# Performance work log

Hardware: AMD Instinct MI355X
Metric: run time of the kernel (lower is better)

Reference implementation:

```python
import jax, jax.numpy as jnp
import numpy as np
import math

INPUT_DIM = 128
HIDDEN = 256
SEQ = 512      # former_seq_len
OUT = 24       # output_dim == number of decode steps
TEMP = 64      # temp_node
B = 512


def setup_inputs() -> dict:
    key = jax.random.key(0)
    ks = jax.random.split(key, 13)
    stdv = 1.0 / math.sqrt(HIDDEN)  # matches init_weights: normal(0, stdv)
    p = lambda k, shape: jax.random.normal(k, shape, dtype=jnp.float32) * stdv
    return {
        "H": jax.random.normal(ks[0], (B, SEQ, INPUT_DIM), dtype=jnp.float32),
        "y_0": jax.random.normal(ks[1], (B, 1), dtype=jnp.float32),
        "embedding": jax.random.normal(ks[2], (B, 2 * HIDDEN), dtype=jnp.float32),
        "Wa": p(ks[3], (INPUT_DIM, OUT, TEMP)),
        "Ua": p(ks[4], (HIDDEN, OUT, TEMP)),
        "ba": p(ks[5], (OUT, TEMP)),
        "Va": p(ks[6], (TEMP, OUT, 1)),
        "W": p(ks[7], (INPUT_DIM, OUT, 4 * HIDDEN)),
        "U": p(ks[8], (HIDDEN, OUT, 4 * HIDDEN)),
        "bias": p(ks[9], (OUT, 4 * HIDDEN)),
        "W_y": p(ks[10], (1, OUT, 4 * HIDDEN)),
        "fc_w": p(ks[11], (OUT, HIDDEN)),   # per-step Linear(hidden,1) weights
        "fc_b": p(ks[12], (OUT, 1)),        # per-step Linear biases
    }


def reference(H, y_0, embedding, Wa, Ua, ba, Va, W, U, bias, W_y, fc_w, fc_b):
    HS = HIDDEN
    scale = 1.0 / math.sqrt(HS)
    h0 = embedding[:, :HS]
    c0 = embedding[:, HS:]
    # stack per-timestep weight slices along a leading T axis for lax.scan
    params = (
        jnp.moveaxis(Wa, 1, 0),   # [T, D, TEMP]
        jnp.moveaxis(Ua, 1, 0),   # [T, HS, TEMP]
        ba,                        # [T, TEMP]
        jnp.moveaxis(Va, 1, 0),   # [T, TEMP, 1]
        jnp.moveaxis(W, 1, 0),    # [T, D, 4HS]
        jnp.moveaxis(U, 1, 0),    # [T, HS, 4HS]
        bias,                      # [T, 4HS]
        jnp.moveaxis(W_y, 1, 0),  # [T, 1, 4HS]
        fc_w,                      # [T, HS]
        fc_b,                      # [T, 1]
    )

    def step(carry, p):
        h_t, c_t, y_prev = carry
        Wa_t, Ua_t, ba_t, Va_t, W_t, U_t, b_t, Wy_t, fcw_t, fcb_t = p
        # additive attention over the encoder sequence (note: uses cell state c_t)
        e = jnp.tanh(H @ Wa_t + (c_t @ Ua_t)[:, None, :] + ba_t) @ Va_t  # [B, L, 1]
        beta = jax.nn.softmax(e[..., 0] * scale, axis=1)                 # [B, L]
        ctx = jnp.einsum('bl,bld->bd', beta, H)                          # [B, D]
        gates = ctx @ W_t + h_t @ U_t + b_t + y_prev @ Wy_t              # [B, 4HS]
        i = jax.nn.sigmoid(gates[:, :HS])
        f = jax.nn.sigmoid(gates[:, HS:2 * HS])
        g = jnp.tanh(gates[:, 2 * HS:3 * HS])
        o = jax.nn.sigmoid(gates[:, 3 * HS:])
        c_new = f * c_t + i * g
        h_new = o * jnp.tanh(c_new)
        y = h_new @ fcw_t[:, None] + fcb_t                                # [B, 1]
        return (h_new, c_new, y), (h_new, y[:, 0])

    _, (hs, ys) = jax.lax.scan(step, (h0, c0, y_0), params)
    y_out = jnp.transpose(ys)            # [B, T]
    hidden_seq = jnp.moveaxis(hs, 0, 1)  # [B, T, HS]
    return y_out, hidden_seq
```

## Files before the change

kernel.cpp:

```cpp
#include <hip/hip_runtime.h>
#include <hip/hip_fp8.h>
#include <cstdint>
#include <cstddef>

#define IDIM 128
#define HS   256
#define SEQL 512
#define TOUT 24
#define TMP  64
#define NB   512
#define G4   1024

typedef unsigned short u16;
typedef unsigned int   u32;
typedef __attribute__((ext_vector_type(4))) float f32x4;
typedef _Float16 f16x8 __attribute__((ext_vector_type(8)));

#define OFF_HFRAG 0
#define OFF_GATEP 65536
#define OFF_E     73728
#define OFF_CUAP  75776
#define OFF_H     77824
#define OFF_C     78848
#define OFF_CTX   79872
#define OFF_CUABA 80384
#define OFF_VA    80640
#define OFF_RED   80896
#define OFF_Y     80992
#define OFF_INVD  80996
#define OFF_AB    81000
#define SMEM_BYTES 81768

__device__ __forceinline__ u16 f2bf(float f) {
  union { float f; u32 u; } v; v.f = f;
  u32 r = v.u + 0x7FFFu + ((v.u >> 16) & 1u);
  return (u16)(r >> 16);
}
__device__ __forceinline__ float bflo(u32 u) {
  union { u32 u; float f; } v; v.u = u << 16; return v.f;
}
__device__ __forceinline__ float bfhi(u32 u) {
  union { u32 u; float f; } v; v.u = u & 0xFFFF0000u; return v.f;
}
__device__ __forceinline__ u32 pkbf(float a, float b) {
  return (u32)f2bf(a) | ((u32)f2bf(b) << 16);
}
__device__ __forceinline__ u32 pkf16(float a, float b) {
  union { _Float16 h[2]; u32 u; } v;
  v.h[0] = (_Float16)a; v.h[1] = (_Float16)b; return v.u;
}
__device__ __forceinline__ u32 pk4_fp8(float a, float b, float c, float d) {
#if __has_builtin(__builtin_amdgcn_cvt_pk_fp8_f32)
  u32 v = (u32)__builtin_amdgcn_cvt_pk_fp8_f32(a, b, 0, false);
  v = (u32)__builtin_amdgcn_cvt_pk_fp8_f32(c, d, (int)v, true);
  return v;
#else
  __hip_fp8_e4m3 x(a), y(b), z(c), w(d);
  return (u32)x.__x | ((u32)y.__x << 8) | ((u32)z.__x << 16) | ((u32)w.__x << 24);
#endif
}
template <int S>
__device__ __forceinline__ float fp8_f32(u32 v) {
#if __has_builtin(__builtin_amdgcn_cvt_f32_fp8)
  return __builtin_amdgcn_cvt_f32_fp8((int)v, S);
#else
  __hip_fp8_e4m3 x; x.__x = (unsigned char)(v >> (8 * S)); return (float)x;
#endif
}
__device__ __forceinline__ float tanh_fast(float x) {
  float x2 = x * x;
  float r = x * (27.0f + x2) * __builtin_amdgcn_rcpf(27.0f + 9.0f * x2);
  return fminf(fmaxf(r, -1.0f), 1.0f);
}
__device__ __forceinline__ float sigmoid_acc(float x) {
  return __builtin_amdgcn_rcpf(1.0f + __builtin_exp2f(-1.4426950408889634f * x));
}
__device__ __forceinline__ float tanh_acc(float x) {
  return 1.0f - 2.0f * __builtin_amdgcn_rcpf(1.0f + __builtin_exp2f(2.8853900817779268f * x));
}

__global__ void repack_f16_kernel(const float* __restrict__ W, const float* __restrict__ U,
                                  u32* __restrict__ WUf) {
  int f = blockIdx.x * blockDim.x + threadIdx.x;
  if (f >= TOUT * 64 * 12 * 64) return;
  int lane = f & 63;
  int kc = (f >> 6) % 12;
  int nt = (f / (64 * 12)) % 64;
  int t = f / (64 * 12 * 64);
  int lm = lane & 15, q = lane >> 4;
  int n = nt * 16 + lm;
  int kb = kc * 32 + q * 8;
  u32 w4[4];
#pragma unroll
  for (int jj = 0; jj < 4; ++jj) {
    int k0 = kb + 2 * jj, k1 = k0 + 1;
    float v0 = (k0 < 128) ? W[((size_t)k0 * TOUT + t) * G4 + n]
                          : U[((size_t)(k0 - 128) * TOUT + t) * G4 + n];
    float v1 = (k1 < 128) ? W[((size_t)k1 * TOUT + t) * G4 + n]
                          : U[((size_t)(k1 - 128) * TOUT + t) * G4 + n];
    w4[jj] = pkf16(v0, v1);
  }
  *(uint4*)(WUf + (size_t)f * 4) = make_uint4(w4[0], w4[1], w4[2], w4[3]);
}

template <int WBF>
__global__ __launch_bounds__(512, 4) void lstm_attn_kernel(
    const float* __restrict__ H, const float* __restrict__ y0, const float* __restrict__ emb,
    const float* __restrict__ Wa, const float* __restrict__ UaF, const float* __restrict__ ba,
    const float* __restrict__ Va, const float* __restrict__ WF, const float* __restrict__ UF,
    const float* __restrict__ bias, const float* __restrict__ WyF, const float* __restrict__ fcw,
    const float* __restrict__ fcb, const u32* __restrict__ WUf, float* __restrict__ out) {
  const int bg = blockIdx.x;
  const int tid = threadIdx.x;
  const int lane = tid & 63;
  const int wv = tid >> 6;
  extern __shared__ char smem[];
  float* eL     = (float*)(smem + OFF_E);
  float* hL     = (float*)(smem + OFF_H);
  float* cL     = (float*)(smem + OFF_C);
  float* ctxL   = (float*)(smem + OFF_CTX);
  float* cuapL  = (float*)(smem + OFF_CUAP);
  float* ctxpL  = (float*)(smem + OFF_CUAP);
  float* cuabaL = (float*)(smem + OFF_CUABA);
  float* vaL    = (float*)(smem + OFF_VA);
  float* redL   = (float*)(smem + OFF_RED);
  float* yL     = (float*)(smem + OFF_Y);
  float* invdL  = (float*)(smem + OFF_INVD);
  u32* gatepU   = (u32*)(smem + OFF_GATEP);
  float* gatesF = (float*)(smem + OFF_GATEP);
  u32* abU      = (u32*)(smem + OFF_AB);

#pragma unroll 2
  for (int it = 0; it < 16; ++it) {
    int ch = it * 512 + tid;
    int l = ch >> 4, oct = ch & 15;
    const float* src = H + (size_t)bg * (SEQL * IDIM) + l * IDIM + oct * 8;
    float4 a = *(const float4*)src;
    float4 c4 = *(const float4*)(src + 4);
    u32 lo = pk4_fp8(a.x, a.y, a.z, a.w);
    u32 hi = pk4_fp8(c4.x, c4.y, c4.z, c4.w);
    int mtile = l >> 4, lm2 = l & 15, kc = oct >> 2, q = oct & 3;
    *(uint2*)(smem + OFF_HFRAG +
              (size_t)(((mtile * 4 + kc) * 64 + q * 16 + lm2)) * 8) = make_uint2(lo, hi);
  }
  if (tid < 256) {
    hL[tid] = emb[(size_t)bg * 512 + tid];
    cL[tid] = emb[(size_t)bg * 512 + 256 + tid];
  }
  if (tid < 128) {
    const float* hp = emb + (size_t)bg * 512 + 2 * tid;
    abU[64 + tid] = pkf16(hp[0], hp[1]);
  }
  if (tid == 0) yL[0] = y0[bg];
  __syncthreads();

#pragma unroll 1
  for (int t = 0; t < TOUT; ++t) {
#pragma unroll
    for (int half = 0; half < 2; ++half) {
      int id = half * 512 + tid;
      int nt = id >> 8, kc = (id >> 6) & 3, l6 = id & 63;
      int lm = l6 & 15, q = l6 >> 4;
      int n = nt * 16 + lm;
      float f[8];
#pragma unroll
      for (int j = 0; j < 8; ++j) {
        int k = kc * 32 + q * 8 + j;
        f[j] = Wa[((size_t)k * TOUT + t) * TMP + n];
      }
      *(uint2*)(smem + OFF_GATEP + (size_t)id * 8) =
          make_uint2(pk4_fp8(f[0], f[1], f[2], f[3]), pk4_fp8(f[4], f[5], f[6], f[7]));
    }
    if (tid < 256) {
      int j2 = tid & 31, part = tid >> 5;
      float s0 = 0.f, s1 = 0.f;
#pragma unroll 8
      for (int i = 0; i < 32; ++i) {
        int d = part * 32 + i;
        const float* up = UaF + ((size_t)d * TOUT + t) * TMP + j2 * 2;
        float c0 = cL[d];
        s0 += c0 * up[0]; s1 += c0 * up[1];
      }
      cuapL[part * 64 + j2 * 2] = s0;
      cuapL[part * 64 + j2 * 2 + 1] = s1;
    }
    if (tid >= 448) vaL[tid - 448] = Va[(size_t)(tid - 448) * TOUT + t];
    __syncthreads();
    if (tid < 64) {
      float s = 0.f;
#pragma unroll
      for (int p = 0; p < 8; ++p) s += cuapL[p * 64 + tid];
      cuabaL[tid] = s + ba[t * TMP + tid];
    }
    __syncthreads();

    {
      const int lm = lane & 15, q = lane >> 4;
      long bfr[4][4];
#pragma unroll
      for (int nt = 0; nt < 4; ++nt)
#pragma unroll
        for (int kc = 0; kc < 4; ++kc)
          bfr[nt][kc] = *(const long*)(smem + OFF_GATEP + (size_t)(((nt * 4 + kc) * 64 + lane)) * 8);
      float cb0 = cuabaL[0 * 16 + lm], cb1 = cuabaL[1 * 16 + lm];
      float cb2 = cuabaL[2 * 16 + lm], cb3 = cuabaL[3 * 16 + lm];
      float vv0 = vaL[0 * 16 + lm], vv1 = vaL[1 * 16 + lm];
      float vv2 = vaL[2 * 16 + lm], vv3 = vaL[3 * 16 + lm];
#pragma unroll
      for (int mm = 0; mm < 4; ++mm) {
        int mtile = wv * 4 + mm;
        f32x4 acc0 = 0, acc1 = 0, acc2 = 0, acc3 = 0;
#pragma unroll
        for (int kc = 0; kc < 4; ++kc) {
          long af = *(const long*)(smem + OFF_HFRAG +
                                   (size_t)(((mtile * 4 + kc) * 64 + lane)) * 8);
          acc0 = __builtin_amdgcn_mfma_f32_16x16x32_fp8_fp8(af, bfr[0][kc], acc0, 0, 0, 0);
          acc1 = __builtin_amdgcn_mfma_f32_16x16x32_fp8_fp8(af, bfr[1][kc], acc1, 0, 0, 0);
          acc2 = __builtin_amdgcn_mfma_f32_16x16x32_fp8_fp8(af, bfr[2][kc], acc2, 0, 0, 0);
          acc3 = __builtin_amdgcn_mfma_f32_16x16x32_fp8_fp8(af, bfr[3][kc], acc3, 0, 0, 0);
        }
#pragma unroll
        for (int r = 0; r < 4; ++r) {
          float v = tanh_fast(acc0[r] + cb0) * vv0 + tanh_fast(acc1[r] + cb1) * vv1 +
                    tanh_fast(acc2[r] + cb2) * vv2 + tanh_fast(acc3[r] + cb3) * vv3;
          v += __shfl_xor(v, 1);
          v += __shfl_xor(v, 2);
          v += __shfl_xor(v, 4);
          v += __shfl_xor(v, 8);
          if (lm == 0) eL[mtile * 16 + q * 4 + r] = v;
        }
      }
    }
    __syncthreads();

    {
      float v = eL[tid];
      float m = v;
#pragma unroll
      for (int msk = 1; msk <= 32; msk <<= 1) m = fmaxf(m, __shfl_xor(m, msk));
      if (lane == 0) redL[wv] = m;
      __syncthreads();
      float M = redL[0];
#pragma unroll
      for (int p = 1; p < 8; ++p) M = fmaxf(M, redL[p]);
      float pv = __builtin_exp2f((v - M) * 0.0901684400347379f);
      eL[tid] = pv;
      float s = pv;
#pragma unroll
      for (int msk = 1; msk <= 32; msk <<= 1) s += __shfl_xor(s, msk);
      if (lane == 0) redL[8 + wv] = s;
      __syncthreads();
      if (tid == 0) {
        float den = redL[8] + redL[9] + redL[10] + redL[11] +
                    redL[12] + redL[13] + redL[14] + redL[15];
        invdL[0] = __builtin_amdgcn_rcpf(den);
      }
    }

    {
      int lsub = tid & 15, dch = (tid >> 4) & 15, half = tid >> 8;
      int kc = dch >> 2, q2 = dch & 3;
      const char* hbase = smem + OFF_HFRAG;
      float a[8] = {0.f, 0.f, 0.f, 0.f, 0.f, 0.f, 0.f, 0.f};
#pragma unroll 4
      for (int i = 0; i < 16; ++i) {
        int mt = half * 16 + i;
        uint2 hv = *(const uint2*)(hbase + (size_t)(((mt * 4 + kc) * 64 + q2 * 16 + lsub)) * 8);
        float p = eL[mt * 16 + lsub];
        a[0] += p * fp8_f32<0>(hv.x); a[1] += p * fp8_f32<1>(hv.x);
        a[2] += p * fp8_f32<2>(hv.x); a[3] += p * fp8_f32<3>(hv.x);
        a[4] += p * fp8_f32<0>(hv.y); a[5] += p * fp8_f32<1>(hv.y);
        a[6] += p * fp8_f32<2>(hv.y); a[7] += p * fp8_f32<3>(hv.y);
      }
#pragma unroll
      for (int msk = 1; msk <= 8; msk <<= 1)
#pragma unroll
        for (int j = 0; j < 8; ++j) a[j] += __shfl_xor(a[j], msk);
      if (lsub == 0) {
        float* dst = &ctxpL[half * 128 + dch * 8];
#pragma unroll
        for (int j = 0; j < 8; ++j) dst[j] = a[j];
      }
    }
    __syncthreads();
    if (tid < 128) {
      float v = (ctxpL[tid] + ctxpL[128 + tid]) * invdL[0];
      ctxL[tid] = v;
      float vo = __shfl_xor(v, 1);
      if (!(tid & 1)) abU[tid >> 1] = pkf16(v, vo);
    }
    __syncthreads();

    if (WBF) {
      const int q = lane >> 4;
      const char* abase = smem + OFF_AB;
#pragma unroll
      for (int half = 0; half < 2; ++half) {
        const f16x8* wb = reinterpret_cast<const f16x8*>(WUf) +
                          ((size_t)t * 64 + wv * 8 + half * 4) * 12 * 64 + lane;
        f32x4 acc0 = 0, acc1 = 0, acc2 = 0, acc3 = 0;
#pragma unroll 4
        for (int kc = 0; kc < 12; ++kc) {
          f16x8 a = *(const f16x8*)(abase + kc * 64 + q * 16);
          const f16x8* bp = wb + (size_t)kc * 64;
          acc0 = __builtin_amdgcn_mfma_f32_16x16x32_f16(a, bp[0], acc0, 0, 0, 0);
          acc1 = __builtin_amdgcn_mfma_f32_16x16x32_f16(a, bp[12 * 64], acc1, 0, 0, 0);
          acc2 = __builtin_amdgcn_mfma_f32_16x16x32_f16(a, bp[2 * 12 * 64], acc2, 0, 0, 0);
          acc3 = __builtin_amdgcn_mfma_f32_16x16x32_f16(a, bp[3 * 12 * 64], acc3, 0, 0, 0);
        }
        if (lane < 16) {
          int c0 = wv * 128 + half * 64 + lane;
          gatesF[c0]      = acc0[0];
          gatesF[c0 + 16] = acc1[0];
          gatesF[c0 + 32] = acc2[0];
          gatesF[c0 + 48] = acc3[0];
        }
      }
    } else {
      int gc = tid & 255, dpart = tid >> 8;
      const int c0 = gc * 4;
      float g0[4] = {0.f, 0.f, 0.f, 0.f};
      {
        const float* wpf = WF + ((size_t)(dpart * 64) * TOUT + t) * G4 + c0;
#pragma unroll 2
        for (int i4 = 0; i4 < 16; ++i4) {
          float4 cv0 = *(const float4*)&ctxL[dpart * 64 + i4 * 4];
#pragma unroll
          for (int j4 = 0; j4 < 4; ++j4) {
            float4 wf = *(const float4*)wpf;
            wpf += (size_t)TOUT * G4;
            float cc0 = (j4 == 0) ? cv0.x : (j4 == 1) ? cv0.y : (j4 == 2) ? cv0.z : cv0.w;
            g0[0] += cc0 * wf.x; g0[1] += cc0 * wf.y; g0[2] += cc0 * wf.z; g0[3] += cc0 * wf.w;
          }
        }
      }
      {
        const float* upf = UF + ((size_t)(dpart * 128) * TOUT + t) * G4 + c0;
#pragma unroll 2
        for (int i4 = 0; i4 < 32; ++i4) {
          float4 hv0 = *(const float4*)&hL[dpart * 128 + i4 * 4];
#pragma unroll
          for (int j4 = 0; j4 < 4; ++j4) {
            float4 wf = *(const float4*)upf;
            upf += (size_t)TOUT * G4;
            float hh0 = (j4 == 0) ? hv0.x : (j4 == 1) ? hv0.y : (j4 == 2) ? hv0.z : hv0.w;
            g0[0] += hh0 * wf.x; g0[1] += hh0 * wf.y; g0[2] += hh0 * wf.z; g0[3] += hh0 * wf.w;
          }
        }
      }
      *(uint2*)&gatepU[dpart * 512 + gc * 2] =
          make_uint2(pkbf(g0[0], g0[1]), pkbf(g0[2], g0[3]));
    }
    __syncthreads();

    float ypart = 0.f;
    if (tid < 256) {
      float yprev = yL[0];
      float gv[4];
#pragma unroll
      for (int gi = 0; gi < 4; ++gi) {
        int col = gi * 256 + tid;
        float s;
        if (WBF) {
          s = gatesF[col];
        } else {
          int ci = col >> 1, sel = col & 1;
          s = 0.f;
#pragma unroll
          for (int p = 0; p < 2; ++p) {
            u32 u = gatepU[p * 512 + ci];
            s += sel ? bfhi(u) : bflo(u);
          }
        }
        s += bias[(size_t)t * G4 + col];
        gv[gi] = s + yprev * WyF[t * G4 + col];
      }
      float ig = sigmoid_acc(gv[0]);
      float fg = sigmoid_acc(gv[1]);
      float gg = tanh_acc(gv[2]);
      float og = sigmoid_acc(gv[3]);
      float cn = fg * cL[tid] + ig * gg;
      float hn = og * tanh_acc(cn);
      cL[tid] = cn;
      hL[tid] = hn;
      out[12288 + ((size_t)bg * TOUT + t) * HS + tid] = hn;
      ypart = hn * fcw[t * HS + tid];
      float hho = __shfl_xor(hn, 1);
      if (!(tid & 1)) abU[64 + (tid >> 1)] = pkf16(hn, hho);
    }
#pragma unroll
    for (int msk = 1; msk <= 32; msk <<= 1) ypart += __shfl_xor(ypart, msk);
    if (tid < 256 && lane == 0) redL[16 + wv] = ypart;
    __syncthreads();
    if (tid == 0) {
      float y = redL[16] + redL[17] + redL[18] + redL[19] + fcb[t];
      yL[0] = y;
      out[(size_t)bg * TOUT + t] = y;
    }
    __syncthreads();
  }
}

extern "C" void kernel_launch(void* const* d_in, const int* in_sizes, int n_in, void* d_out,
                              int out_size, void* d_ws, size_t ws_size, hipStream_t stream) {
  const float* H    = (const float*)d_in[0];
  const float* y0   = (const float*)d_in[1];
  const float* emb  = (const float*)d_in[2];
  const float* Wa   = (const float*)d_in[3];
  const float* Ua   = (const float*)d_in[4];
  const float* ba   = (const float*)d_in[5];
  const float* Va   = (const float*)d_in[6];
  const float* W    = (const float*)d_in[7];
  const float* U    = (const float*)d_in[8];
  const float* bias = (const float*)d_in[9];
  const float* Wy   = (const float*)d_in[10];
  const float* fcw  = (const float*)d_in[11];
  const float* fcb  = (const float*)d_in[12];
  float* out = (float*)d_out;

  const size_t nFrag = (size_t)TOUT * 64 * 12 * 64;
  const size_t need = nFrag * 16;
  const bool usebf = (d_ws != nullptr) && (ws_size >= need);
  u32* WUf = (u32*)d_ws;

  if (usebf) {
    repack_f16_kernel<<<(int)(nFrag / 256), 256, 0, stream>>>(W, U, WUf);
  }

  hipFuncSetAttribute((const void*)lstm_attn_kernel<1>,
                      hipFuncAttributeMaxDynamicSharedMemorySize, SMEM_BYTES);
  hipFuncSetAttribute((const void*)lstm_attn_kernel<0>,
                      hipFuncAttributeMaxDynamicSharedMemorySize, SMEM_BYTES);

  if (usebf) {
    lstm_attn_kernel<1><<<NB, 512, SMEM_BYTES, stream>>>(
        H, y0, emb, Wa, Ua, ba, Va, W, U, bias, Wy, fcw, fcb, WUf, out);
  } else {
    lstm_attn_kernel<0><<<NB, 512, SMEM_BYTES, stream>>>(
        H, y0, emb, Wa, Ua, ba, Va, W, U, bias, Wy, fcw, fcb, WUf, out);
  }
}
```

Measured before the change: 795.9 us.

## Prepack Wa to fp8, split gate GEMM, drop softmax max pass and barriers

Wa is repacked into fp8 MFMA fragments once by a separate kernel, so each step does a plain copy into shared memory instead of a strided gather and convert. The h-part of the gate GEMM (U columns) is issued early into persistent accumulators so it overlaps the attention phase. The ctx part is then added from register-built fp16 fragments. The softmax max-subtraction pass is removed, and the normalisation is folded into the ctx scaling, which removes several barriers and the end-of-step sync. Skipping the max subtraction risks overflow in exp2 if the scores grow large. The persistent accumulators also raise register pressure.

```diff
diff --git a/kernel.cpp b/kernel.cpp
--- a/kernel.cpp
+++ b/kernel.cpp
@@ -103,13 +103,33 @@
   *(uint4*)(WUf + (size_t)f * 4) = make_uint4(w4[0], w4[1], w4[2], w4[3]);
 }
 
+__global__ void repack_wa_kernel(const float* __restrict__ Wa, u32* __restrict__ WaF8) {
+  int f = blockIdx.x * blockDim.x + threadIdx.x;
+  if (f >= TOUT * 16 * 64) return;
+  int lane = f & 63;
+  int fr = (f >> 6) & 15;
+  int t = f >> 10;
+  int nt = fr >> 2, kc = fr & 3;
+  int lm = lane & 15, q = lane >> 4;
+  int n = nt * 16 + lm;
+  float v[8];
+#pragma unroll
+  for (int j = 0; j < 8; ++j) {
+    int k = kc * 32 + q * 8 + j;
+    v[j] = Wa[((size_t)k * TOUT + t) * TMP + n];
+  }
+  *(uint2*)(WaF8 + (size_t)f * 2) =
+      make_uint2(pk4_fp8(v[0], v[1], v[2], v[3]), pk4_fp8(v[4], v[5], v[6], v[7]));
+}
+
 template <int WBF>
 __global__ __launch_bounds__(512, 4) void lstm_attn_kernel(
     const float* __restrict__ H, const float* __restrict__ y0, const float* __restrict__ emb,
     const float* __restrict__ Wa, const float* __restrict__ UaF, const float* __restrict__ ba,
     const float* __restrict__ Va, const float* __restrict__ WF, const float* __restrict__ UF,
     const float* __restrict__ bias, const float* __restrict__ WyF, const float* __restrict__ fcw,
-    const float* __restrict__ fcb, const u32* __restrict__ WUf, float* __restrict__ out) {
+    const float* __restrict__ fcb, const u32* __restrict__ WUf, const u32* __restrict__ WaF8,
+    float* __restrict__ out) {
   const int bg = blockIdx.x;
   const int tid = threadIdx.x;
   const int lane = tid & 63;
@@ -121,11 +141,8 @@
   float* ctxL   = (float*)(smem + OFF_CTX);
   float* cuapL  = (float*)(smem + OFF_CUAP);
   float* ctxpL  = (float*)(smem + OFF_CUAP);
-  float* cuabaL = (float*)(smem + OFF_CUABA);
-  float* vaL    = (float*)(smem + OFF_VA);
   float* redL   = (float*)(smem + OFF_RED);
   float* yL     = (float*)(smem + OFF_Y);
-  float* invdL  = (float*)(smem + OFF_INVD);
   u32* gatepU   = (u32*)(smem + OFF_GATEP);
   float* gatesF = (float*)(smem + OFF_GATEP);
   u32* abU      = (u32*)(smem + OFF_AB);
@@ -156,20 +173,35 @@
 
 #pragma unroll 1
   for (int t = 0; t < TOUT; ++t) {
-#pragma unroll
-    for (int half = 0; half < 2; ++half) {
-      int id = half * 512 + tid;
-      int nt = id >> 8, kc = (id >> 6) & 3, l6 = id & 63;
-      int lm = l6 & 15, q = l6 >> 4;
-      int n = nt * 16 + lm;
-      float f[8];
-#pragma unroll
-      for (int j = 0; j < 8; ++j) {
-        int k = kc * 32 + q * 8 + j;
-        f[j] = Wa[((size_t)k * TOUT + t) * TMP + n];
-      }
-      *(uint2*)(smem + OFF_GATEP + (size_t)id * 8) =
-          make_uint2(pk4_fp8(f[0], f[1], f[2], f[3]), pk4_fp8(f[4], f[5], f[6], f[7]));
+    f32x4 gacc[8];
+#pragma unroll
+    for (int i = 0; i < 8; ++i) gacc[i] = 0;
+
+    if (WBF) {
+      if (tid >= 256) {
+        const uint4* src = (const uint4*)(WaF8 + (size_t)t * 2048);
+        uint4* dst = (uint4*)(smem + OFF_GATEP);
+        int id = tid - 256;
+        dst[id] = src[id];
+        dst[id + 256] = src[id + 256];
+      }
+    } else {
+      if (tid >= 256) {
+        int base = (tid - 256) * 4;
+#pragma unroll
+        for (int ii = 0; ii < 4; ++ii) {
+          int id = base + ii;
+          int nt = id >> 8, kc = (id >> 6) & 3, l6 = id & 63;
+          int lm = l6 & 15, q = l6 >> 4;
+          int n = nt * 16 + lm;
+          float f[8];
+#pragma unroll
+          for (int j = 0; j < 8; ++j)
+            f[j] = Wa[((size_t)(kc * 32 + q * 8 + j) * TOUT + t) * TMP + n];
+          *(uint2*)(smem + OFF_GATEP + (size_t)id * 8) =
+              make_uint2(pk4_fp8(f[0], f[1], f[2], f[3]), pk4_fp8(f[4], f[5], f[6], f[7]));
+        }
+      }
     }
     if (tid < 256) {
       int j2 = tid & 31, part = tid >> 5;
@@ -184,28 +216,34 @@
       cuapL[part * 64 + j2 * 2] = s0;
       cuapL[part * 64 + j2 * 2 + 1] = s1;
     }
-    if (tid >= 448) vaL[tid - 448] = Va[(size_t)(tid - 448) * TOUT + t];
-    __syncthreads();
-    if (tid < 64) {
-      float s = 0.f;
-#pragma unroll
-      for (int p = 0; p < 8; ++p) s += cuapL[p * 64 + tid];
-      cuabaL[tid] = s + ba[t * TMP + tid];
+    if (WBF) {
+      const int q = lane >> 4;
+      const char* abase = smem + OFF_AB;
+#pragma unroll
+      for (int i = 0; i < 8; ++i) {
+        const f16x8* wb = reinterpret_cast<const f16x8*>(WUf) +
+                          ((size_t)t * 64 + wv * 8 + i) * 12 * 64 + lane;
+#pragma unroll
+        for (int kc = 4; kc < 12; ++kc) {
+          f16x8 a = *(const f16x8*)(abase + kc * 64 + q * 16);
+          gacc[i] = __builtin_amdgcn_mfma_f32_16x16x32_f16(a, wb[kc * 64], gacc[i], 0, 0, 0);
+        }
+      }
     }
     __syncthreads();
 
     {
       const int lm = lane & 15, q = lane >> 4;
-      long bfr[4][4];
-#pragma unroll
-      for (int nt = 0; nt < 4; ++nt)
-#pragma unroll
-        for (int kc = 0; kc < 4; ++kc)
-          bfr[nt][kc] = *(const long*)(smem + OFF_GATEP + (size_t)(((nt * 4 + kc) * 64 + lane)) * 8);
-      float cb0 = cuabaL[0 * 16 + lm], cb1 = cuabaL[1 * 16 + lm];
-      float cb2 = cuabaL[2 * 16 + lm], cb3 = cuabaL[3 * 16 + lm];
-      float vv0 = vaL[0 * 16 + lm], vv1 = vaL[1 * 16 + lm];
-      float vv2 = vaL[2 * 16 + lm], vv3 = vaL[3 * 16 + lm];
+      float cb[4], vv[4];
+#pragma unroll
+      for (int nt = 0; nt < 4; ++nt) {
+        float s = 0.f;
+#pragma unroll
+        for (int p = 0; p < 8; ++p) s += cuapL[p * 64 + nt * 16 + lm];
+        cb[nt] = s + ba[t * TMP + nt * 16 + lm];
+        vv[nt] = Va[(size_t)(nt * 16 + lm) * TOUT + t];
+      }
+      float ssum = 0.f;
 #pragma unroll
       for (int mm = 0; mm < 4; ++mm) {
         int mtile = wv * 4 + mm;
@@ -214,48 +252,33 @@
         for (int kc = 0; kc < 4; ++kc) {
           long af = *(const long*)(smem + OFF_HFRAG +
                                    (size_t)(((mtile * 4 + kc) * 64 + lane)) * 8);
-          acc0 = __builtin_amdgcn_mfma_f32_16x16x32_fp8_fp8(af, bfr[0][kc], acc0, 0, 0, 0);
-          acc1 = __builtin_amdgcn_mfma_f32_16x16x32_fp8_fp8(af, bfr[1][kc], acc1, 0, 0, 0);
-          acc2 = __builtin_amdgcn_mfma_f32_16x16x32_fp8_fp8(af, bfr[2][kc], acc2, 0, 0, 0);
-          acc3 = __builtin_amdgcn_mfma_f32_16x16x32_fp8_fp8(af, bfr[3][kc], acc3, 0, 0, 0);
+          long b0 = *(const long*)(smem + OFF_GATEP + (size_t)(((0 * 4 + kc) * 64 + lane)) * 8);
+          long b1 = *(const long*)(smem + OFF_GATEP + (size_t)(((1 * 4 + kc) * 64 + lane)) * 8);
+          long b2 = *(const long*)(smem + OFF_GATEP + (size_t)(((2 * 4 + kc) * 64 + lane)) * 8);
+          long b3 = *(const long*)(smem + OFF_GATEP + (size_t)(((3 * 4 + kc) * 64 + lane)) * 8);
+          acc0 = __builtin_amdgcn_mfma_f32_16x16x32_fp8_fp8(af, b0, acc0, 0, 0, 0);
+          acc1 = __builtin_amdgcn_mfma_f32_16x16x32_fp8_fp8(af, b1, acc1, 0, 0, 0);
+          acc2 = __builtin_amdgcn_mfma_f32_16x16x32_fp8_fp8(af, b2, acc2, 0, 0, 0);
+          acc3 = __builtin_amdgcn_mfma_f32_16x16x32_fp8_fp8(af, b3, acc3, 0, 0, 0);
         }
 #pragma unroll
         for (int r = 0; r < 4; ++r) {
-          float v = tanh_fast(acc0[r] + cb0) * vv0 + tanh_fast(acc1[r] + cb1) * vv1 +
-                    tanh_fast(acc2[r] + cb2) * vv2 + tanh_fast(acc3[r] + cb3) * vv3;
+          float v = tanh_fast(acc0[r] + cb[0]) * vv[0] + tanh_fast(acc1[r] + cb[1]) * vv[1] +
+                    tanh_fast(acc2[r] + cb[2]) * vv[2] + tanh_fast(acc3[r] + cb[3]) * vv[3];
           v += __shfl_xor(v, 1);
           v += __shfl_xor(v, 2);
           v += __shfl_xor(v, 4);
           v += __shfl_xor(v, 8);
-          if (lm == 0) eL[mtile * 16 + q * 4 + r] = v;
-        }
-      }
+          float pv = __builtin_exp2f(v * 0.0901684400347379f);
+          ssum += pv;
+          if (lm == 0) eL[mtile * 16 + q * 4 + r] = pv;
+        }
+      }
+      ssum += __shfl_xor(ssum, 16);
+      ssum += __shfl_xor(ssum, 32);
+      if (lane == 0) redL[wv] = ssum;
     }
     __syncthreads();
-
-    {
-      float v = eL[tid];
-      float m = v;
-#pragma unroll
-      for (int msk = 1; msk <= 32; msk <<= 1) m = fmaxf(m, __shfl_xor(m, msk));
-      if (lane == 0) redL[wv] = m;
-      __syncthreads();
-      float M = redL[0];
-#pragma unroll
-      for (int p = 1; p < 8; ++p) M = fmaxf(M, redL[p]);
-      float pv = __builtin_exp2f((v - M) * 0.0901684400347379f);
-      eL[tid] = pv;
-      float s = pv;
-#pragma unroll
-      for (int msk = 1; msk <= 32; msk <<= 1) s += __shfl_xor(s, msk);
-      if (lane == 0) redL[8 + wv] = s;
-      __syncthreads();
-      if (tid == 0) {
-        float den = redL[8] + redL[9] + redL[10] + redL[11] +
-                    redL[12] + redL[13] + redL[14] + redL[15];
-        invdL[0] = __builtin_amdgcn_rcpf(den);
-      }
-    }
 
     {
       int lsub = tid & 15, dch = (tid >> 4) & 15, half = tid >> 8;
@@ -283,40 +306,42 @@
       }
     }
     __syncthreads();
-    if (tid < 128) {
-      float v = (ctxpL[tid] + ctxpL[128 + tid]) * invdL[0];
-      ctxL[tid] = v;
-      float vo = __shfl_xor(v, 1);
-      if (!(tid & 1)) abU[tid >> 1] = pkf16(v, vo);
-    }
-    __syncthreads();
 
     if (WBF) {
+      float den = redL[0] + redL[1] + redL[2] + redL[3] +
+                  redL[4] + redL[5] + redL[6] + redL[7];
+      float invd = __builtin_amdgcn_rcpf(den);
       const int q = lane >> 4;
-      const char* abase = smem + OFF_AB;
-#pragma unroll
-      for (int half = 0; half < 2; ++half) {
+      f16x8 actx[4];
+#pragma unroll
+      for (int kc = 0; kc < 4; ++kc)
+#pragma unroll
+        for (int j = 0; j < 8; ++j) {
+          int k = kc * 32 + q * 8 + j;
+          actx[kc][j] = (_Float16)((ctxpL[k] + ctxpL[128 + k]) * invd);
+        }
+#pragma unroll
+      for (int i = 0; i < 8; ++i) {
         const f16x8* wb = reinterpret_cast<const f16x8*>(WUf) +
-                          ((size_t)t * 64 + wv * 8 + half * 4) * 12 * 64 + lane;
-        f32x4 acc0 = 0, acc1 = 0, acc2 = 0, acc3 = 0;
-#pragma unroll 4
-        for (int kc = 0; kc < 12; ++kc) {
-          f16x8 a = *(const f16x8*)(abase + kc * 64 + q * 16);
-          const f16x8* bp = wb + (size_t)kc * 64;
-          acc0 = __builtin_amdgcn_mfma_f32_16x16x32_f16(a, bp[0], acc0, 0, 0, 0);
-          acc1 = __builtin_amdgcn_mfma_f32_16x16x32_f16(a, bp[12 * 64], acc1, 0, 0, 0);
-          acc2 = __builtin_amdgcn_mfma_f32_16x16x32_f16(a, bp[2 * 12 * 64], acc2, 0, 0, 0);
-          acc3 = __builtin_amdgcn_mfma_f32_16x16x32_f16(a, bp[3 * 12 * 64], acc3, 0, 0, 0);
-        }
-        if (lane < 16) {
-          int c0 = wv * 128 + half * 64 + lane;
-          gatesF[c0]      = acc0[0];
-          gatesF[c0 + 16] = acc1[0];
-          gatesF[c0 + 32] = acc2[0];
-          gatesF[c0 + 48] = acc3[0];
-        }
+                          ((size_t)t * 64 + wv * 8 + i) * 12 * 64 + lane;
+#pragma unroll
+        for (int kc = 0; kc < 4; ++kc)
+          gacc[i] = __builtin_amdgcn_mfma_f32_16x16x32_f16(actx[kc], wb[kc * 64], gacc[i],
+                                                           0, 0, 0);
+      }
+      if (lane < 16) {
+#pragma unroll
+        for (int i = 0; i < 8; ++i)
+          gatesF[(wv * 8 + i) * 16 + lane] = gacc[i][0];
       }
     } else {
+      if (tid < 128) {
+        float den = redL[0] + redL[1] + redL[2] + redL[3] +
+                    redL[4] + redL[5] + redL[6] + redL[7];
+        float invd = __builtin_amdgcn_rcpf(den);
+        ctxL[tid] = (ctxpL[tid] + ctxpL[128 + tid]) * invd;
+      }
+      __syncthreads();
       int gc = tid & 255, dpart = tid >> 8;
       const int c0 = gc * 4;
       float g0[4] = {0.f, 0.f, 0.f, 0.f};
@@ -382,7 +407,7 @@
       float cn = fg * cL[tid] + ig * gg;
       float hn = og * tanh_acc(cn);
       cL[tid] = cn;
-      hL[tid] = hn;
+      if (!WBF) hL[tid] = hn;
       out[12288 + ((size_t)bg * TOUT + t) * HS + tid] = hn;
       ypart = hn * fcw[t * HS + tid];
       float hho = __shfl_xor(hn, 1);
@@ -397,7 +422,6 @@
       yL[0] = y;
       out[(size_t)bg * TOUT + t] = y;
     }
-    __syncthreads();
   }
 }
 
@@ -419,12 +443,15 @@
   float* out = (float*)d_out;
 
   const size_t nFrag = (size_t)TOUT * 64 * 12 * 64;
-  const size_t need = nFrag * 16;
+  const size_t nWaFrag = (size_t)TOUT * 16 * 64;
+  const size_t need = nFrag * 16 + nWaFrag * 8;
   const bool usebf = (d_ws != nullptr) && (ws_size >= need);
   u32* WUf = (u32*)d_ws;
+  u32* WaF8 = WUf + nFrag * 4;
 
   if (usebf) {
     repack_f16_kernel<<<(int)(nFrag / 256), 256, 0, stream>>>(W, U, WUf);
+    repack_wa_kernel<<<(int)(nWaFrag / 256), 256, 0, stream>>>(Wa, WaF8);
   }
 
   hipFuncSetAttribute((const void*)lstm_attn_kernel<1>,
@@ -434,9 +461,9 @@
 
   if (usebf) {
     lstm_attn_kernel<1><<<NB, 512, SMEM_BYTES, stream>>>(
-        H, y0, emb, Wa, Ua, ba, Va, W, U, bias, Wy, fcw, fcb, WUf, out);
+        H, y0, emb, Wa, Ua, ba, Va, W, U, bias, Wy, fcw, fcb, WUf, WaF8, out);
   } else {
     lstm_attn_kernel<0><<<NB, 512, SMEM_BYTES, stream>>>(
-        H, y0, emb, Wa, Ua, ba, Va, W, U, bias, Wy, fcw, fcb, WUf, out);
-  }
-}
+        H, y0, emb, Wa, Ua, ba, Va, W, U, bias, Wy, fcw, fcb, WUf, WaF8, out);
+  }
+}
```

New measurement: 1.196 ms. +50.3%, slower.
